# Kernel optimization log

Measured on AMD Instinct MI355X. Metric: run time of the kernel, lower is better.

## Reference

```python
import jax, jax.numpy as jnp
import numpy as np

DIM, N_HEAD, DK, DV = 1024, 16, 64, 64
B, S = 1, 4096


def setup_inputs() -> dict:
    key = jax.random.key(0)
    ks = jax.random.split(key, 9)
    sd = 0.02
    return {
        "x": jax.random.normal(ks[0], (B, S, DIM), dtype=jnp.float32),
        "Wq": jax.random.normal(ks[1], (DIM, N_HEAD * DK), dtype=jnp.float32) * sd,
        "bq": jnp.zeros((N_HEAD * DK,), dtype=jnp.float32),
        "Wk": jax.random.normal(ks[2], (DIM, N_HEAD * DK), dtype=jnp.float32) * sd,
        "bk": jnp.zeros((N_HEAD * DK,), dtype=jnp.float32),
        "Wv": jax.random.normal(ks[3], (DIM, N_HEAD * DV), dtype=jnp.float32) * sd,
        "bv": jnp.zeros((N_HEAD * DV,), dtype=jnp.float32),
        "Wo": jax.random.normal(ks[4], (N_HEAD * DV, DIM), dtype=jnp.float32) * sd,
        "bo": jnp.zeros((DIM,), dtype=jnp.float32),
    }


def reference(x, Wq, bq, Wk, bk, Wv, bv, Wo, bo):
    b, s, _ = x.shape
    scale = DK ** (-0.5)
    # projections -> [b, h, s, d]
    q = (x @ Wq + bq).reshape(b, s, N_HEAD, DK).transpose(0, 2, 1, 3)
    k = (x @ Wk + bk).reshape(b, s, N_HEAD, DK).transpose(0, 2, 1, 3)
    v = (x @ Wv + bv).reshape(b, s, N_HEAD, DV).transpose(0, 2, 1, 3)
    attn = jnp.einsum("bhqd,bhkd->bhqk", q, k) * scale  # [b,h,s,s]
    attn = jax.nn.softmax(attn, axis=-1)
    out = jnp.einsum("bhqk,bhkd->bhqd", attn, v)  # [b,h,s,dv]
    out = out.transpose(0, 2, 1, 3).reshape(b, s, N_HEAD * DV)
    return out @ Wo + bo
```

## Files before the change

kernel.cpp:

```cpp
#include <hip/hip_runtime.h>
#include <hip/hip_bf16.h>
#include <hip/hip_fp16.h>

#define SEQ 4096
#define DIM 1024
#define NH 16
#define NT (SEQ / 64)

typedef __attribute__((ext_vector_type(4))) float f32x4;
typedef __attribute__((ext_vector_type(16))) float f32x16;
typedef __attribute__((ext_vector_type(8))) _Float16 half8;
typedef __attribute__((ext_vector_type(4))) _Float16 half4;

#if __has_builtin(__builtin_amdgcn_exp2f)
#define EXP2(x) __builtin_amdgcn_exp2f(x)
#else
#define EXP2(x) exp2f(x)
#endif

#define SMC 0.18033688f

__global__ __launch_bounds__(256) void prep_all(const float* __restrict__ x,
                                                _Float16* __restrict__ xh,
                                                const float* __restrict__ W0,
                                                const float* __restrict__ W1,
                                                const float* __restrict__ W2,
                                                const float* __restrict__ W3,
                                                _Float16* __restrict__ T0,
                                                _Float16* __restrict__ T1,
                                                _Float16* __restrict__ T2,
                                                _Float16* __restrict__ T3) {
  if (blockIdx.z == 4) {
    const int blkid = blockIdx.x * 32 + blockIdx.y;
#pragma unroll
    for (int u = 0; u < 4; u++) {
      int i = blkid * 4096 + u * 1024 + threadIdx.x * 4;
      float4 v = *reinterpret_cast<const float4*>(x + i);
      half4 h;
      h[0] = (_Float16)v.x; h[1] = (_Float16)v.y;
      h[2] = (_Float16)v.z; h[3] = (_Float16)v.w;
      *reinterpret_cast<half4*>(xh + i) = h;
    }
    return;
  }
  const float* W = blockIdx.z == 0 ? W0 : blockIdx.z == 1 ? W1 : blockIdx.z == 2 ? W2 : W3;
  _Float16* Wt = blockIdx.z == 0 ? T0 : blockIdx.z == 1 ? T1 : blockIdx.z == 2 ? T2 : T3;
  __shared__ float t[32][33];
  int bx = blockIdx.x * 32;
  int by = blockIdx.y * 32;
  int tx = threadIdx.x & 31, ty = threadIdx.x >> 5;
#pragma unroll
  for (int i = 0; i < 4; i++)
    t[ty + i * 8][tx] = W[(by + ty + i * 8) * DIM + bx + tx];
  __syncthreads();
#pragma unroll
  for (int i = 0; i < 4; i++)
    Wt[(bx + ty + i * 8) * DIM + by + tx] = (_Float16)t[tx][ty + i * 8];
}

template <int MODE>
__device__ __forceinline__ void gemm_body(const _Float16* __restrict__ A,
                                          const _Float16* __restrict__ Bt,
                                          const float* __restrict__ bias,
                                          void* __restrict__ outp,
                                          int M, int N, int Kd, int bmb, int bnb) {
  __shared__ __align__(16) _Float16 As[64][72];
  __shared__ __align__(16) _Float16 Bs[128][72];
  const int tid = threadIdx.x, lane = tid & 63, w = tid >> 6;
  const int bm = bmb * 64, bn = bnb * 128;
  const int l15 = lane & 15, g = lane >> 4, kb = g * 8;
  const int sra = tid >> 2, sca = (tid & 3) * 16;
  const int srb = tid >> 1, scb = (tid & 1) * 32;
  f32x4 acc[4][2] = {};

  uint4 ar0, ar1, br0, br1, br2, br3;
  auto LOADT = [&](int k0) {
    const _Float16* ap = A + (size_t)(bm + sra) * Kd + k0 + sca;
    ar0 = *reinterpret_cast<const uint4*>(ap);
    ar1 = *reinterpret_cast<const uint4*>(ap + 8);
    const _Float16* bp = Bt + (size_t)(bn + srb) * Kd + k0 + scb;
    br0 = *reinterpret_cast<const uint4*>(bp);
    br1 = *reinterpret_cast<const uint4*>(bp + 8);
    br2 = *reinterpret_cast<const uint4*>(bp + 16);
    br3 = *reinterpret_cast<const uint4*>(bp + 24);
  };

  LOADT(0);
  for (int k0 = 0; k0 < Kd; k0 += 64) {
    __syncthreads();
    *reinterpret_cast<uint4*>(&As[sra][sca]) = ar0;
    *reinterpret_cast<uint4*>(&As[sra][sca + 8]) = ar1;
    *reinterpret_cast<uint4*>(&Bs[srb][scb]) = br0;
    *reinterpret_cast<uint4*>(&Bs[srb][scb + 8]) = br1;
    *reinterpret_cast<uint4*>(&Bs[srb][scb + 16]) = br2;
    *reinterpret_cast<uint4*>(&Bs[srb][scb + 24]) = br3;
    __syncthreads();
    if (k0 + 64 < Kd) LOADT(k0 + 64);
#pragma unroll
    for (int kk = 0; kk < 64; kk += 32) {
      half8 af[4], bf[2];
#pragma unroll
      for (int i = 0; i < 4; i++)
        af[i] = *reinterpret_cast<const half8*>(&As[i * 16 + l15][kk + kb]);
#pragma unroll
      for (int j = 0; j < 2; j++)
        bf[j] = *reinterpret_cast<const half8*>(&Bs[w * 32 + j * 16 + l15][kk + kb]);
      __builtin_amdgcn_s_setprio(1);
#pragma unroll
      for (int i = 0; i < 4; i++)
#pragma unroll
        for (int j = 0; j < 2; j++)
          acc[i][j] = __builtin_amdgcn_mfma_f32_16x16x32_f16(af[i], bf[j], acc[i][j], 0, 0, 0);
      __builtin_amdgcn_s_setprio(0);
    }
  }

  const int gswap = ((g & 1) << 1) | (g >> 1);
#pragma unroll
  for (int i = 0; i < 4; i++)
#pragma unroll
    for (int j = 0; j < 2; j++) {
      const int col = bn + w * 32 + j * 16 + l15;
      if (MODE == 2) {
        const int rowP = bm + i * 16 + gswap * 4;
        half4 hv;
#pragma unroll
        for (int r = 0; r < 4; r++) hv[r] = (_Float16)(acc[i][j][r] + bias[col]);
        *reinterpret_cast<half4*>(&((_Float16*)outp)[(size_t)col * M + rowP]) = hv;
      } else {
        const int row0 = bm + i * 16 + g * 4;
#pragma unroll
        for (int r = 0; r < 4; r++) {
          float vv = acc[i][j][r] + bias[col];
          if (MODE == 0) {
            _Float16* O = (_Float16*)outp;
            O[(((col >> 6) * SEQ) + row0 + r) * 64 + (col & 63)] = (_Float16)vv;
          } else {
            float* O = (float*)outp;
            O[(size_t)(row0 + r) * N + col] = vv;
          }
        }
      }
    }
}

__global__ __launch_bounds__(256) void gemm_qkv(const _Float16* __restrict__ A,
                                                const _Float16* __restrict__ WqT,
                                                const _Float16* __restrict__ WkT,
                                                const _Float16* __restrict__ WvT,
                                                const float* __restrict__ bq,
                                                const float* __restrict__ bk,
                                                const float* __restrict__ bv,
                                                _Float16* __restrict__ Qd,
                                                _Float16* __restrict__ Kd,
                                                _Float16* __restrict__ Vd) {
  if (blockIdx.z == 0)
    gemm_body<0>(A, WqT, bq, (void*)Qd, SEQ, DIM, DIM, blockIdx.x, blockIdx.y);
  else if (blockIdx.z == 1)
    gemm_body<0>(A, WkT, bk, (void*)Kd, SEQ, DIM, DIM, blockIdx.x, blockIdx.y);
  else
    gemm_body<2>(A, WvT, bv, (void*)Vd, SEQ, DIM, DIM, blockIdx.x, blockIdx.y);
}

__global__ __launch_bounds__(256) void gemm_out(const _Float16* __restrict__ A,
                                                const _Float16* __restrict__ Bt,
                                                const float* __restrict__ bias,
                                                float* __restrict__ out) {
  gemm_body<1>(A, Bt, bias, (void*)out, SEQ, DIM, DIM, blockIdx.x, blockIdx.y);
}

__global__ __launch_bounds__(256) void attn_fwd(const _Float16* __restrict__ Q,
                                                const _Float16* __restrict__ Kh,
                                                const _Float16* __restrict__ Vt_g,
                                                _Float16* __restrict__ Og) {
  __shared__ __align__(16) _Float16 Ks[3][64][72];
  __shared__ __align__(16) _Float16 Vs[3][64][72];
  const int hh = blockIdx.y;
  const int q0 = blockIdx.x * 128;
  const int tid = threadIdx.x, lane = tid & 63, w = tid >> 6;
  const int l31 = lane & 31, hq = lane >> 5, h8 = hq * 8;

  const int qrow = q0 + w * 32 + l31;
  const _Float16* qp = Q + ((size_t)hh * SEQ + qrow) * 64;
  half8 qf[4];
#pragma unroll
  for (int d = 0; d < 4; d++)
    qf[d] = *reinterpret_cast<const half8*>(qp + d * 16 + h8);

  f32x16 o[2] = {};
  float m = -1e30f, lsum = 0.f, negmC = 1e30f;
  const f32x16 kZero16 = {};

  const int srow = tid >> 3, sc8 = (tid & 7) * 8;
  const _Float16* kbase = Kh + (size_t)hh * SEQ * 64;
  const _Float16* vbase = Vt_g + (size_t)hh * 64 * SEQ;

  uint4 kr0, kr1, vr0, vr1;
  auto LOADKV = [&](int kt2) {
    const _Float16* kp = kbase + (size_t)(kt2 * 64 + srow) * 64 + sc8;
    kr0 = *reinterpret_cast<const uint4*>(kp);
    kr1 = *reinterpret_cast<const uint4*>(kp + 32 * 64);
    const _Float16* vp = vbase + (size_t)srow * SEQ + kt2 * 64 + sc8;
    vr0 = *reinterpret_cast<const uint4*>(vp);
    vr1 = *reinterpret_cast<const uint4*>(vp + 32 * SEQ);
  };
  auto STAGE = [&](int buf) {
    *reinterpret_cast<uint4*>(&Ks[buf][srow][sc8]) = kr0;
    *reinterpret_cast<uint4*>(&Ks[buf][srow + 32][sc8]) = kr1;
    *reinterpret_cast<uint4*>(&Vs[buf][srow][sc8]) = vr0;
    *reinterpret_cast<uint4*>(&Vs[buf][srow + 32][sc8]) = vr1;
  };

  auto QK = [&](int tile, f32x16 (&sf)[2]) {
    const int b = tile % 3;
    __builtin_amdgcn_s_setprio(1);
    {
      half8 kf0 = *reinterpret_cast<const half8*>(&Ks[b][l31][h8]);
      half8 kf1 = *reinterpret_cast<const half8*>(&Ks[b][32 + l31][h8]);
      sf[0] = __builtin_amdgcn_mfma_f32_32x32x16_f16(kf0, qf[0], kZero16, 0, 0, 0);
      sf[1] = __builtin_amdgcn_mfma_f32_32x32x16_f16(kf1, qf[0], kZero16, 0, 0, 0);
    }
#pragma unroll
    for (int d = 1; d < 4; d++) {
      half8 kf0 = *reinterpret_cast<const half8*>(&Ks[b][l31][d * 16 + h8]);
      half8 kf1 = *reinterpret_cast<const half8*>(&Ks[b][32 + l31][d * 16 + h8]);
      sf[0] = __builtin_amdgcn_mfma_f32_32x32x16_f16(kf0, qf[d], sf[0], 0, 0, 0);
      sf[1] = __builtin_amdgcn_mfma_f32_32x32x16_f16(kf1, qf[d], sf[1], 0, 0, 0);
    }
    __builtin_amdgcn_s_setprio(0);
  };

  auto ITER = [&](int t, f32x16 (&scur)[2], f32x16 (&snext)[2]) {
    if (t + 1 < NT) QK(t + 1, snext);

    float t0 = fmaxf(fmaxf(scur[0][0], scur[0][1]), scur[0][2]);
    float t1 = fmaxf(fmaxf(scur[0][3], scur[0][4]), scur[0][5]);
    float t2 = fmaxf(fmaxf(scur[0][6], scur[0][7]), scur[0][8]);
    float t3 = fmaxf(fmaxf(scur[0][9], scur[0][10]), scur[0][11]);
    float t4 = fmaxf(fmaxf(scur[0][12], scur[0][13]), scur[0][14]);
    float t5 = fmaxf(fmaxf(scur[0][15], scur[1][0]), scur[1][1]);
    float t6 = fmaxf(fmaxf(scur[1][2], scur[1][3]), scur[1][4]);
    float t7 = fmaxf(fmaxf(scur[1][5], scur[1][6]), scur[1][7]);
    float t8 = fmaxf(fmaxf(scur[1][8], scur[1][9]), scur[1][10]);
    float t9 = fmaxf(fmaxf(scur[1][11], scur[1][12]), scur[1][13]);
    float ta = fmaxf(scur[1][14], scur[1][15]);
    float u0 = fmaxf(fmaxf(t0, t1), t2);
    float u1 = fmaxf(fmaxf(t3, t4), t5);
    float u2 = fmaxf(fmaxf(t6, t7), t8);
    float u3 = fmaxf(t9, ta);
    float pm = fmaxf(fmaxf(fmaxf(u0, u1), u2), u3);

    if (__any(pm > m + 64.f)) {
      pm = fmaxf(pm, __shfl_xor(pm, 32, 64));
      float mn = fmaxf(m, pm);
      float al = EXP2((m - mn) * SMC);
      m = mn;
      negmC = -mn * SMC;
      lsum *= al;
      o[0] *= al;
      o[1] *= al;
    }
    f32x16 pf0, pf1;
#pragma unroll
    for (int r = 0; r < 16; r++) {
      float p = EXP2(fmaf(scur[0][r], SMC, negmC));
      pf0[r] = p;
      lsum += p;
    }
#pragma unroll
    for (int r = 0; r < 16; r++) {
      float p = EXP2(fmaf(scur[1][r], SMC, negmC));
      pf1[r] = p;
      lsum += p;
    }
    half8 pb[4];
#pragma unroll
    for (int s = 0; s < 4; s++) {
      const int base = (s & 1) * 8;
      unsigned d0, d1, d2, d3;
      if (s < 2) {
        d0 = __builtin_bit_cast(unsigned, __builtin_amdgcn_cvt_pkrtz(pf0[base + 0], pf0[base + 1]));
        d1 = __builtin_bit_cast(unsigned, __builtin_amdgcn_cvt_pkrtz(pf0[base + 2], pf0[base + 3]));
        d2 = __builtin_bit_cast(unsigned, __builtin_amdgcn_cvt_pkrtz(pf0[base + 4], pf0[base + 5]));
        d3 = __builtin_bit_cast(unsigned, __builtin_amdgcn_cvt_pkrtz(pf0[base + 6], pf0[base + 7]));
      } else {
        d0 = __builtin_bit_cast(unsigned, __builtin_amdgcn_cvt_pkrtz(pf1[base + 0], pf1[base + 1]));
        d1 = __builtin_bit_cast(unsigned, __builtin_amdgcn_cvt_pkrtz(pf1[base + 2], pf1[base + 3]));
        d2 = __builtin_bit_cast(unsigned, __builtin_amdgcn_cvt_pkrtz(pf1[base + 4], pf1[base + 5]));
        d3 = __builtin_bit_cast(unsigned, __builtin_amdgcn_cvt_pkrtz(pf1[base + 6], pf1[base + 7]));
      }
      uint4 uu = {d0, d1, d2, d3};
      pb[s] = __builtin_bit_cast(half8, uu);
    }

    const int bv = t % 3;
    __builtin_amdgcn_s_setprio(1);
#pragma unroll
    for (int s = 0; s < 4; s++) {
      half8 va0 = *reinterpret_cast<const half8*>(&Vs[bv][l31][s * 16 + h8]);
      half8 va1 = *reinterpret_cast<const half8*>(&Vs[bv][32 + l31][s * 16 + h8]);
      o[0] = __builtin_amdgcn_mfma_f32_32x32x16_f16(va0, pb[s], o[0], 0, 0, 0);
      o[1] = __builtin_amdgcn_mfma_f32_32x32x16_f16(va1, pb[s], o[1], 0, 0, 0);
    }
    __builtin_amdgcn_s_setprio(0);

    if (t + 2 < NT) STAGE((t + 2) % 3);
    if (t + 3 < NT) LOADKV(t + 3);
    __syncthreads();
  };

  LOADKV(0); STAGE(0);
  LOADKV(1); STAGE(1);
  LOADKV(2);
  __syncthreads();

  f32x16 sfA[2], sfB[2];
  QK(0, sfA);
  for (int t = 0; t < NT; t += 2) {
    ITER(t, sfA, sfB);
    ITER(t + 1, sfB, sfA);
  }

  float ls = lsum + __shfl_xor(lsum, 32, 64);
  float rinv = 1.f / ls;
#pragma unroll
  for (int tile = 0; tile < 2; tile++)
#pragma unroll
    for (int rg = 0; rg < 4; rg++) {
      half4 hv;
#pragma unroll
      for (int j = 0; j < 4; j++) hv[j] = (_Float16)(o[tile][rg * 4 + j] * rinv);
      const int dv = tile * 32 + rg * 8 + 4 * hq;
      *reinterpret_cast<half4*>(&Og[(size_t)qrow * DIM + hh * 64 + dv]) = hv;
    }
}


extern "C" void kernel_launch(void* const* d_in, const int* in_sizes, int n_in,
                              void* d_out, int out_size, void* d_ws, size_t ws_size,
                              hipStream_t stream) {
  const float* x  = (const float*)d_in[0];
  const float* Wq = (const float*)d_in[1];
  const float* bq = (const float*)d_in[2];
  const float* Wk = (const float*)d_in[3];
  const float* bk = (const float*)d_in[4];
  const float* Wv = (const float*)d_in[5];
  const float* bv = (const float*)d_in[6];
  const float* Wo = (const float*)d_in[7];
  const float* bo = (const float*)d_in[8];

  char* ws = (char*)d_ws;
  _Float16* xh  = (_Float16*)ws;
  _Float16* WqT = (_Float16*)(ws + (size_t)SEQ * DIM * 2);
  _Float16* WkT = WqT + DIM * DIM;
  _Float16* WvT = WkT + DIM * DIM;
  _Float16* WoT = WvT + DIM * DIM;
  _Float16* Qd  = WoT + DIM * DIM;
  _Float16* Kd  = Qd + (size_t)SEQ * DIM;
  _Float16* Vd  = Kd + (size_t)SEQ * DIM;
  _Float16* Od  = Vd + (size_t)SEQ * DIM;

  prep_all<<<dim3(32, 32, 5), 256, 0, stream>>>(x, xh, Wq, Wk, Wv, Wo,
                                                WqT, WkT, WvT, WoT);

  gemm_qkv<<<dim3(SEQ / 64, DIM / 128, 3), 256, 0, stream>>>(
      xh, WqT, WkT, WvT, bq, bk, bv, Qd, Kd, Vd);

  attn_fwd<<<dim3(SEQ / 128, NH), 256, 0, stream>>>(Qd, Kd, Vd, Od);

  gemm_out<<<dim3(SEQ / 64, DIM / 128), 256, 0, stream>>>(Od, WoT, bo, (float*)d_out);
}
```

Baseline: 171.8 us.

## Use direct global-to-LDS loads with 128x128 GEMM tiles

Rewrites the shared GEMM body to load A and B tiles with global_load_lds straight into LDS, bypassing registers. The tile grows from 64x128 to 128x128 with a 2x2 warp layout and a 4x4 MFMA accumulator per warp, and K steps shrink from 64 to 32. This aims to raise data reuse per tile and cut register staging. In exchange it drops the register prefetch double-buffering, so loads are no longer overlapped with compute, and the unpadded LDS rows may cause bank conflicts. Grids halve to 256 blocks for the output GEMM.

```diff
diff --git a/kernel.cpp b/kernel.cpp
--- a/kernel.cpp
+++ b/kernel.cpp
@@ -11,6 +11,9 @@
 typedef __attribute__((ext_vector_type(16))) float f32x16;
 typedef __attribute__((ext_vector_type(8))) _Float16 half8;
 typedef __attribute__((ext_vector_type(4))) _Float16 half4;
+
+typedef const unsigned __attribute__((address_space(1)))* gas_t;
+typedef unsigned __attribute__((address_space(3)))* las_t;
 
 #if __has_builtin(__builtin_amdgcn_exp2f)
 #define EXP2(x) __builtin_amdgcn_exp2f(x)
@@ -64,71 +67,60 @@
                                           const float* __restrict__ bias,
                                           void* __restrict__ outp,
                                           int M, int N, int Kd, int bmb, int bnb) {
-  __shared__ __align__(16) _Float16 As[64][72];
-  __shared__ __align__(16) _Float16 Bs[128][72];
+  __shared__ __align__(16) _Float16 As[128][32];
+  __shared__ __align__(16) _Float16 Bs[128][32];
   const int tid = threadIdx.x, lane = tid & 63, w = tid >> 6;
-  const int bm = bmb * 64, bn = bnb * 128;
+  const int bm = bmb * 128, bn = bnb * 128;
   const int l15 = lane & 15, g = lane >> 4, kb = g * 8;
-  const int sra = tid >> 2, sca = (tid & 3) * 16;
-  const int srb = tid >> 1, scb = (tid & 1) * 32;
-  f32x4 acc[4][2] = {};
-
-  uint4 ar0, ar1, br0, br1, br2, br3;
-  auto LOADT = [&](int k0) {
-    const _Float16* ap = A + (size_t)(bm + sra) * Kd + k0 + sca;
-    ar0 = *reinterpret_cast<const uint4*>(ap);
-    ar1 = *reinterpret_cast<const uint4*>(ap + 8);
-    const _Float16* bp = Bt + (size_t)(bn + srb) * Kd + k0 + scb;
-    br0 = *reinterpret_cast<const uint4*>(bp);
-    br1 = *reinterpret_cast<const uint4*>(bp + 8);
-    br2 = *reinterpret_cast<const uint4*>(bp + 16);
-    br3 = *reinterpret_cast<const uint4*>(bp + 24);
-  };
-
-  LOADT(0);
-  for (int k0 = 0; k0 < Kd; k0 += 64) {
+  const int wr = (w >> 1) * 64, wc = (w & 1) * 64;
+  const int lr = lane >> 2;
+  const int lc = (lane & 3) * 8;
+  f32x4 acc[4][4] = {};
+
+  for (int k0 = 0; k0 < Kd; k0 += 32) {
     __syncthreads();
-    *reinterpret_cast<uint4*>(&As[sra][sca]) = ar0;
-    *reinterpret_cast<uint4*>(&As[sra][sca + 8]) = ar1;
-    *reinterpret_cast<uint4*>(&Bs[srb][scb]) = br0;
-    *reinterpret_cast<uint4*>(&Bs[srb][scb + 8]) = br1;
-    *reinterpret_cast<uint4*>(&Bs[srb][scb + 16]) = br2;
-    *reinterpret_cast<uint4*>(&Bs[srb][scb + 24]) = br3;
+    const _Float16* as0 = A + (size_t)(bm + w * 32 + lr) * Kd + k0 + lc;
+    __builtin_amdgcn_global_load_lds((gas_t)(const void*)as0,
+                                     (las_t)(void*)&As[w * 32][0], 16, 0, 0);
+    __builtin_amdgcn_global_load_lds((gas_t)(const void*)(as0 + (size_t)16 * Kd),
+                                     (las_t)(void*)&As[w * 32 + 16][0], 16, 0, 0);
+    const _Float16* bs0 = Bt + (size_t)(bn + w * 32 + lr) * Kd + k0 + lc;
+    __builtin_amdgcn_global_load_lds((gas_t)(const void*)bs0,
+                                     (las_t)(void*)&Bs[w * 32][0], 16, 0, 0);
+    __builtin_amdgcn_global_load_lds((gas_t)(const void*)(bs0 + (size_t)16 * Kd),
+                                     (las_t)(void*)&Bs[w * 32 + 16][0], 16, 0, 0);
     __syncthreads();
-    if (k0 + 64 < Kd) LOADT(k0 + 64);
-#pragma unroll
-    for (int kk = 0; kk < 64; kk += 32) {
-      half8 af[4], bf[2];
-#pragma unroll
-      for (int i = 0; i < 4; i++)
-        af[i] = *reinterpret_cast<const half8*>(&As[i * 16 + l15][kk + kb]);
-#pragma unroll
-      for (int j = 0; j < 2; j++)
-        bf[j] = *reinterpret_cast<const half8*>(&Bs[w * 32 + j * 16 + l15][kk + kb]);
-      __builtin_amdgcn_s_setprio(1);
-#pragma unroll
-      for (int i = 0; i < 4; i++)
-#pragma unroll
-        for (int j = 0; j < 2; j++)
-          acc[i][j] = __builtin_amdgcn_mfma_f32_16x16x32_f16(af[i], bf[j], acc[i][j], 0, 0, 0);
-      __builtin_amdgcn_s_setprio(0);
-    }
+
+    half8 af[4], bf[4];
+#pragma unroll
+    for (int i = 0; i < 4; i++)
+      af[i] = *reinterpret_cast<const half8*>(&As[wr + i * 16 + l15][kb]);
+#pragma unroll
+    for (int j = 0; j < 4; j++)
+      bf[j] = *reinterpret_cast<const half8*>(&Bs[wc + j * 16 + l15][kb]);
+    __builtin_amdgcn_s_setprio(1);
+#pragma unroll
+    for (int i = 0; i < 4; i++)
+#pragma unroll
+      for (int j = 0; j < 4; j++)
+        acc[i][j] = __builtin_amdgcn_mfma_f32_16x16x32_f16(af[i], bf[j], acc[i][j], 0, 0, 0);
+    __builtin_amdgcn_s_setprio(0);
   }
 
   const int gswap = ((g & 1) << 1) | (g >> 1);
 #pragma unroll
   for (int i = 0; i < 4; i++)
 #pragma unroll
-    for (int j = 0; j < 2; j++) {
-      const int col = bn + w * 32 + j * 16 + l15;
+    for (int j = 0; j < 4; j++) {
+      const int col = bn + wc + j * 16 + l15;
       if (MODE == 2) {
-        const int rowP = bm + i * 16 + gswap * 4;
+        const int rowP = bm + wr + i * 16 + gswap * 4;
         half4 hv;
 #pragma unroll
         for (int r = 0; r < 4; r++) hv[r] = (_Float16)(acc[i][j][r] + bias[col]);
         *reinterpret_cast<half4*>(&((_Float16*)outp)[(size_t)col * M + rowP]) = hv;
       } else {
-        const int row0 = bm + i * 16 + g * 4;
+        const int row0 = bm + wr + i * 16 + g * 4;
 #pragma unroll
         for (int r = 0; r < 4; r++) {
           float vv = acc[i][j][r] + bias[col];
@@ -363,10 +355,10 @@
   prep_all<<<dim3(32, 32, 5), 256, 0, stream>>>(x, xh, Wq, Wk, Wv, Wo,
                                                 WqT, WkT, WvT, WoT);
 
-  gemm_qkv<<<dim3(SEQ / 64, DIM / 128, 3), 256, 0, stream>>>(
+  gemm_qkv<<<dim3(SEQ / 128, DIM / 128, 3), 256, 0, stream>>>(
       xh, WqT, WkT, WvT, bq, bk, bv, Qd, Kd, Vd);
 
   attn_fwd<<<dim3(SEQ / 128, NH), 256, 0, stream>>>(Qd, Kd, Vd, Od);
 
-  gemm_out<<<dim3(SEQ / 64, DIM / 128), 256, 0, stream>>>(Od, WoT, bo, (float*)d_out);
-}
+  gemm_out<<<dim3(SEQ / 128, DIM / 128), 256, 0, stream>>>(Od, WoT, bo, (float*)d_out);
+}
```

Measured after the change: 172.6 us. Within noise of the previous version (+0.5%).
